# Performance work log

Measured on AMD Instinct MI355X. Metric: run time of the kernel, lower is better.

## Reference

```python
import jax, jax.numpy as jnp
import numpy as np

N, C, SUBVEC, K, DOUT, DEPTH = 16384, 64, 16, 16, 1024, 4


def setup_inputs() -> dict:
    key = jax.random.key(0)
    k1, k2, k3, k4, k5 = jax.random.split(key, 5)
    x = jax.random.normal(k1, (N, C * SUBVEC), dtype=jnp.float32)
    split_idxs = jax.random.randint(k2, (C, DEPTH), 0, SUBVEC, dtype=jnp.int32)
    split_vals = jax.random.normal(k3, (C, DEPTH, K // 2), dtype=jnp.float32)
    lookup_tables = jax.random.normal(k4, (C, K, DOUT), dtype=jnp.float32)
    bias = jax.random.normal(k5, (DOUT,), dtype=jnp.float32)
    return {"x": x, "split_idxs": split_idxs, "split_vals": split_vals,
            "lookup_tables": lookup_tables, "bias": bias}


def _encode(x_sub, split_idxs, split_vals):
    # x_sub: (n, C, subvec_len); split_idxs: (C, 4); split_vals: (C, 4, 8)
    n = x_sub.shape[0]
    c_idx = jnp.arange(C)
    enc = jnp.zeros((n, C), dtype=jnp.int32)
    for t in range(DEPTH):  # fixed tree depth 4
        xv = x_sub[:, c_idx, split_idxs[:, t]]            # (n, C) selected feature per codebook
        thresh = split_vals[c_idx[None, :], t, enc]       # (n, C) per-node threshold
        enc = 2 * enc + (xv > thresh).astype(jnp.int32)
    return enc  # values in [0, 16)


def reference(x, split_idxs, split_vals, lookup_tables, bias):
    n = x.shape[0]
    x_sub = x.reshape(n, C, SUBVEC)
    enc = _encode(x_sub, split_idxs, split_vals)           # (n, C) int32
    onehot = jax.nn.one_hot(enc, K, dtype=x.dtype)         # (n, C, K)
    out = jnp.einsum('nck,cko->no', onehot, lookup_tables) # sum over codebooks of LUT rows
    return out + bias
```

## Files before the change

kernel.cpp:

```cpp
#include <hip/hip_runtime.h>

#define NN    16384
#define CBN   64
#define SUBV  16
#define KCODE 16
#define DOUTN 1024
#define DEP   4

typedef short bf16x8 __attribute__((ext_vector_type(8)));
typedef float f32x16 __attribute__((ext_vector_type(16)));

static __device__ __forceinline__ unsigned short f2bf(float f) {
  unsigned int u = __float_as_uint(f);
  u += 0x7FFFu + ((u >> 16) & 1u);
  return (unsigned short)(u >> 16);
}

static __device__ __forceinline__ void gld16(const void* g, void* l) {
  __builtin_amdgcn_global_load_lds(
      (const __attribute__((address_space(1))) unsigned int*)g,
      (__attribute__((address_space(3))) unsigned int*)(uintptr_t)l, 16, 0, 0);
}

__global__ __launch_bounds__(256) void prep_k(
    const float* __restrict__ x, const int* __restrict__ split_idxs,
    const float* __restrict__ split_vals, const float* __restrict__ Tg,
    unsigned char* __restrict__ codes, unsigned int* __restrict__ Tswz) {
  const int t = threadIdx.x;

  if (blockIdx.x < 64) {
    const int img = blockIdx.x;
    const int g = img >> 3, ch = img & 7;
    unsigned int* dst = Tswz + (size_t)img * 8192;
    const int colq = t & 31, kp = (t >> 5) & 7;
    #pragma unroll
    for (int cl = 0; cl < 8; ++cl) {
      const float* g0 = Tg + ((size_t)((ch * 8 + cl) * KCODE + 2 * kp)) * DOUTN
                        + g * 128 + colq * 4;
      float4 r0 = *(const float4*)g0;
      float4 r1 = *(const float4*)(g0 + DOUTN);
      unsigned int pk[4] = {
        f2bf(r0.x) | ((unsigned int)f2bf(r1.x) << 16),
        f2bf(r0.y) | ((unsigned int)f2bf(r1.y) << 16),
        f2bf(r0.z) | ((unsigned int)f2bf(r1.z) << 16),
        f2bf(r0.w) | ((unsigned int)f2bf(r1.w) << 16)};
      unsigned key = (unsigned)(colq & 7) << 2;
      #pragma unroll
      for (int j = 0; j < 4; ++j)
        dst[cl * 1024 + ((((unsigned)(colq * 4 + j)) * 8 + (unsigned)kp) ^ key)]
            = pk[j];
    }
    return;
  }

  __shared__ __align__(16) float xs[8][SUBV * CBN];
  __shared__ int   sidxT[DEP * CBN];
  __shared__ float svalT[DEP * (KCODE / 2) * CBN];
  if (t < DEP * CBN) {
    int d = t >> 6, c = t & 63;
    sidxT[t] = split_idxs[c * DEP + d];
  }
  for (int i = t; i < DEP * (KCODE / 2) * CBN; i += 256) {
    int c = i & 63, de = i >> 6, d = de >> 3, e = de & 7;
    svalT[i] = split_vals[(c * DEP + d) * (KCODE / 2) + e];
  }
  const int n0 = (blockIdx.x - 64) * 8;
  const float4* xg = (const float4*)(x + (size_t)n0 * DOUTN);
  #pragma unroll
  for (int i = 0; i < 8; ++i) {
    int li = t + i * 256;
    int r = li >> 8, cpos = li & 255;
    float4 v = xg[r * 256 + cpos];
    int c = cpos >> 2, q = cpos & 3;
    *(float4*)&xs[r][c * SUBV + ((q ^ (c & 3)) << 2)] = v;
  }
  __syncthreads();
  const int c = t & 63, rg = t >> 6;
  #pragma unroll
  for (int i = 0; i < 2; ++i) {
    int nl = rg * 2 + i;
    int e = 0;
    #pragma unroll
    for (int d = 0; d < DEP; ++d) {
      int si = sidxT[d * 64 + c];
      float xv = xs[nl][c * SUBV + (((si >> 2) ^ (c & 3)) << 2) + (si & 3)];
      float th = svalT[(d * 8 + e) * 64 + c];
      e = 2 * e + (xv > th ? 1 : 0);
    }
    codes[(size_t)(n0 + nl) * CBN + c] = (unsigned char)e;
  }
}

__global__ __launch_bounds__(1024, 4) void maddness_mfma(
    const unsigned int* __restrict__ Tswz, const float* __restrict__ bias,
    const unsigned char* __restrict__ codes, float* __restrict__ out) {
  __shared__ __align__(16) unsigned int Tb[32768];

  const int t = threadIdx.x;
  const int wid = t >> 6, lane = t & 63, lrow = lane & 31, h = lane >> 5;
  const int g16 = blockIdx.x, g8 = g16 >> 1, half = g16 & 1;
  const int n0 = blockIdx.y * 1024;
  const char* img = (const char*)Tswz + (size_t)g8 * 8 * 32768;

  #pragma unroll
  for (int i = 0; i < 8; ++i) {
    int gs = wid * 8 + i;
    int ch = gs >> 4, s16 = gs & 15, cl = s16 >> 1, pc = s16 & 1;
    gld16(img + ch * 32768 + cl * 4096 + half * 2048 + pc * 1024 + lane * 16,
          (char*)Tb + gs * 1024);
  }

  f32x16 acc[2][2];
  #pragma unroll
  for (int rt = 0; rt < 2; ++rt)
    #pragma unroll
    for (int ct = 0; ct < 2; ++ct)
      #pragma unroll
      for (int e = 0; e < 16; ++e) acc[rt][ct][e] = 0.f;

  const unsigned char* crow = codes + (size_t)(n0 + wid * 64 + lrow) * CBN;
  unsigned long long qwA[2], qwB[2];
  qwA[0] = *(const unsigned long long*)(crow);
  qwA[1] = *(const unsigned long long*)(crow + 32 * CBN);

  __syncthreads();

  #pragma unroll
  for (int ch = 0; ch < 8; ++ch) {
    if (ch < 7) {
      qwB[0] = *(const unsigned long long*)(crow + (ch + 1) * 8);
      qwB[1] = *(const unsigned long long*)(crow + 32 * CBN + (ch + 1) * 8);
    }
    const unsigned short* tb = (const unsigned short*)Tb + ch * 8192;
    __builtin_amdgcn_s_setprio(1);
    #pragma unroll
    for (int cl = 0; cl < 8; ++cl) {
      bf16x8 bv[2];
      #pragma unroll
      for (int ct = 0; ct < 2; ++ct) {
        unsigned col_loc = (unsigned)(ct * 32 + lrow);
        unsigned uidx = (unsigned)(cl * 1024)
                      + ((col_loc * 16 + (unsigned)h * 8)
                         ^ (((col_loc >> 2) & 7u) << 3));
        bv[ct] = *(const bf16x8*)(tb + uidx);
      }
      #pragma unroll
      for (int rt = 0; rt < 2; ++rt) {
        int c = (int)((qwA[rt] >> (8 * cl)) & 255);
        int p = c >> 1;
        unsigned s = 0x3F80u << ((c & 1) << 4);
        union { unsigned int u[4]; bf16x8 v; } A;
        #pragma unroll
        for (int j = 0; j < 4; ++j) A.u[j] = (p == h * 4 + j) ? s : 0u;
        acc[rt][0] = __builtin_amdgcn_mfma_f32_32x32x16_bf16(A.v, bv[0], acc[rt][0], 0, 0, 0);
        acc[rt][1] = __builtin_amdgcn_mfma_f32_32x32x16_bf16(A.v, bv[1], acc[rt][1], 0, 0, 0);
      }
    }
    __builtin_amdgcn_s_setprio(0);
    qwA[0] = qwB[0]; qwA[1] = qwB[1];
  }

  #pragma unroll
  for (int ct = 0; ct < 2; ++ct) {
    const int col = g16 * 64 + ct * 32 + lrow;
    const float bval = bias[col];
    #pragma unroll
    for (int rt = 0; rt < 2; ++rt)
      #pragma unroll
      for (int r = 0; r < 16; ++r) {
        int row = n0 + wid * 64 + rt * 32 + (r & 3) + 8 * (r >> 2) + 4 * h;
        out[(size_t)row * DOUTN + col] = acc[rt][ct][r] + bval;
      }
  }
}

extern "C" void kernel_launch(void* const* d_in, const int* in_sizes, int n_in,
                              void* d_out, int out_size, void* d_ws, size_t ws_size,
                              hipStream_t stream) {
  const float* x    = (const float*)d_in[0];
  const int*   sidx = (const int*)d_in[1];
  const float* sval = (const float*)d_in[2];
  const float* Tg   = (const float*)d_in[3];
  const float* bias = (const float*)d_in[4];
  float* out = (float*)d_out;
  unsigned char* codes = (unsigned char*)d_ws;
  unsigned int*  Tswz  = (unsigned int*)((char*)d_ws + (1 << 20));

  prep_k<<<64 + NN / 8, 256, 0, stream>>>(x, sidx, sval, Tg, codes, Tswz);
  maddness_mfma<<<dim3(16, 16), 1024, 0, stream>>>(Tswz, bias, codes, out);
}
```

Measured before the change: 52.82 us.

## Stagger chunk order per wave, software-pipeline LDS B loads, fold bias into accumulator

Each wave now starts its chunk loop at a wave-dependent offset, which spreads LDS bank and port pressure across waves. B-fragment LDS reads are prefetched one step ahead in a register pipeline, with precomputed swizzle offsets. One-hot A construction is simplified to 64-bit selects. Bias is loaded up front and used as the initial accumulator value, which removes the add in the epilogue. The setprio hints are dropped, and the extra live registers could reduce occupancy under the 1024-thread launch bound.

```diff
diff --git a/kernel.cpp b/kernel.cpp
--- a/kernel.cpp
+++ b/kernel.cpp
@@ -110,66 +110,77 @@
           (char*)Tb + gs * 1024);
   }
 
+  const float bv0 = bias[g16 * 64 + lrow];
+  const float bv1 = bias[g16 * 64 + 32 + lrow];
+
   f32x16 acc[2][2];
   #pragma unroll
   for (int rt = 0; rt < 2; ++rt)
     #pragma unroll
-    for (int ct = 0; ct < 2; ++ct)
-      #pragma unroll
-      for (int e = 0; e < 16; ++e) acc[rt][ct][e] = 0.f;
-
-  const unsigned char* crow = codes + (size_t)(n0 + wid * 64 + lrow) * CBN;
-  unsigned long long qwA[2], qwB[2];
-  qwA[0] = *(const unsigned long long*)(crow);
-  qwA[1] = *(const unsigned long long*)(crow + 32 * CBN);
+    for (int e = 0; e < 16; ++e) { acc[rt][0][e] = bv0; acc[rt][1][e] = bv1; }
+
+  const unsigned char* crow0 = codes + (size_t)(n0 + wid * 64 + lrow) * CBN;
+  const unsigned char* crow1 = crow0 + 32 * CBN;
+  const unsigned h2 = 2u * (unsigned)h, h2p = h2 + 1u;
+  const unsigned rb0 = ((unsigned)lrow * 16 + (unsigned)h * 8)
+                     ^ ((((unsigned)lrow >> 2) & 7u) << 3);
+  const unsigned cl32 = (unsigned)lrow + 32u;
+  const unsigned rb1 = (cl32 * 16 + (unsigned)h * 8)
+                     ^ (((cl32 >> 2) & 7u) << 3);
 
   __syncthreads();
 
-  #pragma unroll
-  for (int ch = 0; ch < 8; ++ch) {
-    if (ch < 7) {
-      qwB[0] = *(const unsigned long long*)(crow + (ch + 1) * 8);
-      qwB[1] = *(const unsigned long long*)(crow + 32 * CBN + (ch + 1) * 8);
-    }
-    const unsigned short* tb = (const unsigned short*)Tb + ch * 8192;
-    __builtin_amdgcn_s_setprio(1);
+  const int ch0 = wid & 7;
+  unsigned long long qA0 = *(const unsigned long long*)(crow0 + ch0 * 8);
+  unsigned long long qA1 = *(const unsigned long long*)(crow1 + ch0 * 8);
+  const unsigned short* tbc = (const unsigned short*)Tb + ch0 * 8192;
+  bf16x8 bP0 = *(const bf16x8*)(tbc + rb0);
+  bf16x8 bP1 = *(const bf16x8*)(tbc + rb1);
+
+  #pragma unroll
+  for (int i = 0; i < 8; ++i) {
+    const int chn = (wid + i + 1) & 7;
+    const unsigned short* tbn = (const unsigned short*)Tb + chn * 8192;
+    const unsigned long long q0 = qA0, q1 = qA1;
+    if (i < 7) {
+      qA0 = *(const unsigned long long*)(crow0 + chn * 8);
+      qA1 = *(const unsigned long long*)(crow1 + chn * 8);
+    }
     #pragma unroll
     for (int cl = 0; cl < 8; ++cl) {
-      bf16x8 bv[2];
-      #pragma unroll
-      for (int ct = 0; ct < 2; ++ct) {
-        unsigned col_loc = (unsigned)(ct * 32 + lrow);
-        unsigned uidx = (unsigned)(cl * 1024)
-                      + ((col_loc * 16 + (unsigned)h * 8)
-                         ^ (((col_loc >> 2) & 7u) << 3));
-        bv[ct] = *(const bf16x8*)(tb + uidx);
+      const bf16x8 b0 = bP0, b1 = bP1;
+      if (!(i == 7 && cl == 7)) {
+        const unsigned short* tnx = (cl == 7) ? tbn : (tbc + (cl + 1) * 1024);
+        bP0 = *(const bf16x8*)(tnx + rb0);
+        bP1 = *(const bf16x8*)(tnx + rb1);
       }
       #pragma unroll
       for (int rt = 0; rt < 2; ++rt) {
-        int c = (int)((qwA[rt] >> (8 * cl)) & 255);
-        int p = c >> 1;
-        unsigned s = 0x3F80u << ((c & 1) << 4);
-        union { unsigned int u[4]; bf16x8 v; } A;
-        #pragma unroll
-        for (int j = 0; j < 4; ++j) A.u[j] = (p == h * 4 + j) ? s : 0u;
-        acc[rt][0] = __builtin_amdgcn_mfma_f32_32x32x16_bf16(A.v, bv[0], acc[rt][0], 0, 0, 0);
-        acc[rt][1] = __builtin_amdgcn_mfma_f32_32x32x16_bf16(A.v, bv[1], acc[rt][1], 0, 0, 0);
+        const unsigned q32 =
+            (unsigned)((rt ? q1 : q0) >> ((cl & 4) ? 32 : 0));
+        const unsigned bpos = 8u * (unsigned)(cl & 3);
+        const unsigned sh  = (q32 >> bpos) & 3u;
+        const unsigned key = (q32 >> (bpos + 2)) & 3u;
+        const unsigned long long tt = 0x3F80ULL << (sh << 4);
+        union { unsigned long long q[2]; bf16x8 v; } A;
+        A.q[0] = (key == h2)  ? tt : 0ULL;
+        A.q[1] = (key == h2p) ? tt : 0ULL;
+        acc[rt][0] = __builtin_amdgcn_mfma_f32_32x32x16_bf16(A.v, b0, acc[rt][0], 0, 0, 0);
+        acc[rt][1] = __builtin_amdgcn_mfma_f32_32x32x16_bf16(A.v, b1, acc[rt][1], 0, 0, 0);
       }
     }
-    __builtin_amdgcn_s_setprio(0);
-    qwA[0] = qwB[0]; qwA[1] = qwB[1];
+    tbc = tbn;
   }
 
   #pragma unroll
   for (int ct = 0; ct < 2; ++ct) {
     const int col = g16 * 64 + ct * 32 + lrow;
-    const float bval = bias[col];
     #pragma unroll
     for (int rt = 0; rt < 2; ++rt)
       #pragma unroll
       for (int r = 0; r < 16; ++r) {
         int row = n0 + wid * 64 + rt * 32 + (r & 3) + 8 * (r >> 2) + 4 * h;
-        out[(size_t)row * DOUTN + col] = acc[rt][ct][r] + bval;
+        out[(size_t)row * DOUTN + col] = acc[rt][ct][r];
       }
   }
 }
```

After: 51.90 us. About the same (-1.7%).
